# Kernel optimization log

Hardware: AMD Instinct MI355X
Metric: run time of the kernel (lower is better)

Reference implementation:

```python
import jax, jax.numpy as jnp
import numpy as np

B, T, H = 2, 512, 256


def setup_inputs() -> dict:
    key = jax.random.key(0)
    k1, k2, k3, k4, k5 = jax.random.split(key, 5)
    scale = 1.0 / np.sqrt(H)
    Q = jax.random.normal(k1, (B, T, H), dtype=jnp.float32)
    K = jax.random.normal(k2, (B, T, H), dtype=jnp.float32)
    # torch nn.Linear weights: y = x @ W.T, W shape [out, in]
    Wq = jax.random.normal(k3, (H, H), dtype=jnp.float32) * scale
    Wk = jax.random.normal(k4, (H, H), dtype=jnp.float32) * scale
    v = jax.random.normal(k5, (H,), dtype=jnp.float32) * scale  # Linear(H,1) weight
    return {"Q": Q, "K": K, "Wq": Wq, "Wk": Wk, "v": v}


def reference(Q, K, Wq, Wk, v):
    # Project queries and keys: [B,T,H]
    Qp = jnp.einsum("bth,oh->bto", Q, Wq)
    Kp = jnp.einsum("bsh,oh->bso", K, Wk)
    # Additive (Bahdanau) scores: tanh over broadcast sum -> [B,T,T,H], then v-proj -> [B,T,T]
    e = jnp.tanh(Qp[:, :, None, :] + Kp[:, None, :, :])
    scores = jnp.einsum("btsh,h->bts", e, v)
    # Causal mask: query t may only attend to keys s <= t
    mask = jnp.tril(jnp.ones((T, T), dtype=bool))
    scores = jnp.where(mask[None, :, :], scores, jnp.float32(-1e9))
    alpha = jax.nn.softmax(scores, axis=-1)
    # Weighted sum of (raw) K values: [B,T,H]
    ctx = jnp.einsum("bts,bsh->bth", alpha, K)
    return ctx, alpha
```

## Files before the change

kernel.cpp:

```cpp
#include <hip/hip_runtime.h>

#define BB 2
#define TT 512
#define HH 256
#define NBT (BB * TT)

#define C2LOG2E 2.8853900817779268f
#define LOG2E   1.4426950408889634f

__global__ __launch_bounds__(256) void prep_T(
    const float* __restrict__ Wq, const float* __restrict__ Wk,
    float* __restrict__ WqT, float* __restrict__ WkT)
{
    int bid = blockIdx.x;
    int tid = threadIdx.x;
    const float* W = (bid < 16) ? Wq : Wk;
    float* WT = (bid < 16) ? WqT : WkT;
    int tile = bid & 15;
    int o0 = (tile >> 2) * 64, h0 = (tile & 3) * 64;
    __shared__ float t_sh[64][65];
    int ty = tid >> 6, tx = tid & 63;
#pragma unroll
    for (int r = 0; r < 16; ++r) {
        int o = r * 4 + ty;
        t_sh[o][tx] = W[(o0 + o) * HH + h0 + tx];
    }
    __syncthreads();
#pragma unroll
    for (int r = 0; r < 16; ++r) {
        int h = r * 4 + ty;
        WT[(h0 + h) * HH + o0 + tx] = t_sh[tx][h];
    }
}

__global__ __launch_bounds__(256) void proj_outer(
    const float* __restrict__ Q, const float* __restrict__ K,
    const float* __restrict__ WqT, const float* __restrict__ WkT,
    float* __restrict__ Eq, float* __restrict__ EkT)
{
    __shared__ float x_sh[8][HH];
    __shared__ float ek_sh[4][8][68];

    int bid = blockIdx.x;
    bool isK = (bid >= 128);
    int bt0 = (bid & 127) * 8;
    const float* X = isK ? K : Q;
    const float* WT = isK ? WkT : WqT;
    int tid = threadIdx.x;
    int wv = tid >> 6, lane = tid & 63;
    int o = wv * 64 + lane;

#pragma unroll
    for (int p = 0; p < 2; ++p) {
        int fi = p * 256 + tid;
        int r = fi >> 6, c = fi & 63;
        *reinterpret_cast<float4*>(&x_sh[r][c * 4]) =
            *reinterpret_cast<const float4*>(X + (bt0 + r) * HH + c * 4);
    }
    __syncthreads();

    float acc[8] = {0.f, 0.f, 0.f, 0.f, 0.f, 0.f, 0.f, 0.f};
    const float* wcol = WT + o;
#pragma unroll 2
    for (int h4 = 0; h4 < 64; ++h4) {
        float w0 = wcol[(h4 * 4 + 0) * HH];
        float w1 = wcol[(h4 * 4 + 1) * HH];
        float w2 = wcol[(h4 * 4 + 2) * HH];
        float w3 = wcol[(h4 * 4 + 3) * HH];
#pragma unroll
        for (int r = 0; r < 8; ++r) {
            float4 x4 = *reinterpret_cast<const float4*>(&x_sh[r][h4 * 4]);
            float a = acc[r];
            a = __builtin_fmaf(x4.x, w0, a);
            a = __builtin_fmaf(x4.y, w1, a);
            a = __builtin_fmaf(x4.z, w2, a);
            a = __builtin_fmaf(x4.w, w3, a);
            acc[r] = a;
        }
    }

    float e[8];
#pragma unroll
    for (int r = 0; r < 8; ++r)
        e[r] = __builtin_amdgcn_exp2f(acc[r] * C2LOG2E);

    if (!isK) {
#pragma unroll
        for (int r = 0; r < 8; ++r)
            Eq[(bt0 + r) * HH + o] = e[r];
    } else {
#pragma unroll
        for (int r = 0; r < 8; ++r)
            ek_sh[wv][r][lane] = e[r];
#pragma unroll
        for (int p = 0; p < 2; ++p) {
            int id = p * 64 + lane;
            int s = id >> 3, r = id & 7;
            float4 val = *reinterpret_cast<const float4*>(&ek_sh[wv][r][s * 4]);
            *reinterpret_cast<float4*>(
                EkT + ((wv * 16 + s) * NBT + bt0 + r) * 4) = val;
        }
    }
}

__global__ __launch_bounds__(512, 8) void attn_kernel(
    const float* __restrict__ Eq, const float* __restrict__ EkT,
    const float* __restrict__ Kraw, const float* __restrict__ v,
    float* __restrict__ ctx, float* __restrict__ alpha)
{
    __shared__ float eq_sh[HH];
    __shared__ float v2_sh[HH];
    __shared__ float al_sh[TT];
    __shared__ float red[8];
    __shared__ float4 cred[8][64];

    int bt = blockIdx.x;
    int b = bt / TT;
    int idx = bt % TT;
    int t = (idx < 256) ? idx : 767 - idx;
    int btr = b * TT + t;
    int tid = threadIdx.x;

    if (tid < HH) {
        eq_sh[tid] = Eq[btr * HH + tid];
        v2_sh[tid] = -2.0f * v[tid];
    }
    __syncthreads();

    float sc = 0.f;
    if (tid <= t) {
        const float4* ek = reinterpret_cast<const float4*>(EkT) + (b * TT + tid);
        const float4* q4p = reinterpret_cast<const float4*>(eq_sh);
        const float4* v4p = reinterpret_cast<const float4*>(v2_sh);
#pragma unroll 4
        for (int h4 = 0; h4 < HH / 4; ++h4) {
            float4 e4 = ek[h4 * NBT];
            float4 q4 = q4p[h4];
            float4 vv = v4p[h4];
            float r0 = __builtin_amdgcn_rcpf(__builtin_fmaf(q4.x, e4.x, 1.f));
            float r1 = __builtin_amdgcn_rcpf(__builtin_fmaf(q4.y, e4.y, 1.f));
            float r2 = __builtin_amdgcn_rcpf(__builtin_fmaf(q4.z, e4.z, 1.f));
            float r3 = __builtin_amdgcn_rcpf(__builtin_fmaf(q4.w, e4.w, 1.f));
            sc = __builtin_fmaf(vv.x, r0, sc);
            sc = __builtin_fmaf(vv.y, r1, sc);
            sc = __builtin_fmaf(vv.z, r2, sc);
            sc = __builtin_fmaf(vv.w, r3, sc);
        }
    }

    float e = (tid <= t) ? __builtin_amdgcn_exp2f(sc * LOG2E) : 0.f;
    float ssum = e;
#pragma unroll
    for (int off = 32; off > 0; off >>= 1)
        ssum += __shfl_xor(ssum, off);
    if ((tid & 63) == 0) red[tid >> 6] = ssum;
    __syncthreads();
    float denom = (red[0] + red[1]) + (red[2] + red[3])
                + (red[4] + red[5]) + (red[6] + red[7]);
    float a0 = e * __builtin_amdgcn_rcpf(denom);

    al_sh[tid] = a0;
    alpha[btr * TT + tid] = a0;
    __syncthreads();

    int hc = tid & 63, sg = tid >> 6;
    const float4* kb4 = reinterpret_cast<const float4*>(Kraw + b * TT * HH) + hc;
    float4 acc4 = {0.f, 0.f, 0.f, 0.f};
    for (int s = sg; s <= t; s += 8) {
        float4 k4 = kb4[s * 64];
        float  al = al_sh[s];
        acc4.x = __builtin_fmaf(al, k4.x, acc4.x);
        acc4.y = __builtin_fmaf(al, k4.y, acc4.y);
        acc4.z = __builtin_fmaf(al, k4.z, acc4.z);
        acc4.w = __builtin_fmaf(al, k4.w, acc4.w);
    }
    cred[sg][hc] = acc4;
    __syncthreads();
    if (sg == 0) {
        float4 out = {0.f, 0.f, 0.f, 0.f};
#pragma unroll
        for (int g = 0; g < 8; ++g) {
            float4 cc = cred[g][hc];
            out.x += cc.x; out.y += cc.y; out.z += cc.z; out.w += cc.w;
        }
        reinterpret_cast<float4*>(ctx + btr * HH)[hc] = out;
    }
}

extern "C" void kernel_launch(void* const* d_in, const int* in_sizes, int n_in,
                              void* d_out, int out_size, void* d_ws, size_t ws_size,
                              hipStream_t stream) {
    const float* Q  = (const float*)d_in[0];
    const float* K  = (const float*)d_in[1];
    const float* Wq = (const float*)d_in[2];
    const float* Wk = (const float*)d_in[3];
    const float* v  = (const float*)d_in[4];

    float* ctx   = (float*)d_out;
    float* alpha = (float*)d_out + NBT * HH;

    float* Eq  = (float*)d_ws;
    float* EkT = Eq + NBT * HH;
    float* WqT = EkT + NBT * HH;
    float* WkT = WqT + HH * HH;

    prep_T<<<32, 256, 0, stream>>>(Wq, Wk, WqT, WkT);
    proj_outer<<<256, 256, 0, stream>>>(Q, K, WqT, WkT, Eq, EkT);
    attn_kernel<<<NBT, 512, 0, stream>>>(Eq, EkT, K, v, ctx, alpha);
}
```

Before: 45.87 us.

## Retile projection kernel to 4 rows per block with float4 weight loads

Restructures the projection GEMM so each block handles 4 rows instead of 8 and each thread computes 4 adjacent output columns for one row, loading weights as float4. Grid doubles to 512 blocks, giving more parallelism across CUs for this small GEMM. The trade-off is less reuse of each weight load across rows, which increases total weight traffic from L2. The EkT transpose store is simplified to match the new tiling.

Result: slower. 51.73 us (+12.8%).

```diff
diff --git a/kernel.cpp b/kernel.cpp
--- a/kernel.cpp
+++ b/kernel.cpp
@@ -33,73 +33,71 @@
     }
 }
 
-__global__ __launch_bounds__(256) void proj_outer(
+__global__ __launch_bounds__(256) void proj2_kernel(
     const float* __restrict__ Q, const float* __restrict__ K,
     const float* __restrict__ WqT, const float* __restrict__ WkT,
     float* __restrict__ Eq, float* __restrict__ EkT)
 {
-    __shared__ float x_sh[8][HH];
-    __shared__ float ek_sh[4][8][68];
+    __shared__ float x_sh[4][HH];
+    __shared__ float ek_sh[4][HH + 4];
 
     int bid = blockIdx.x;
-    bool isK = (bid >= 128);
-    int bt0 = (bid & 127) * 8;
+    bool isK = (bid >= 256);
+    int bt0 = (bid & 255) * 4;
     const float* X = isK ? K : Q;
     const float* WT = isK ? WkT : WqT;
     int tid = threadIdx.x;
-    int wv = tid >> 6, lane = tid & 63;
-    int o = wv * 64 + lane;
-
-#pragma unroll
-    for (int p = 0; p < 2; ++p) {
-        int fi = p * 256 + tid;
-        int r = fi >> 6, c = fi & 63;
+    int q = tid & 63;
+    int rg = tid >> 6;
+
+    {
+        int r = tid >> 6, c = tid & 63;
         *reinterpret_cast<float4*>(&x_sh[r][c * 4]) =
             *reinterpret_cast<const float4*>(X + (bt0 + r) * HH + c * 4);
     }
     __syncthreads();
 
-    float acc[8] = {0.f, 0.f, 0.f, 0.f, 0.f, 0.f, 0.f, 0.f};
-    const float* wcol = WT + o;
-#pragma unroll 2
+    float4 acc = {0.f, 0.f, 0.f, 0.f};
+    const float* wbase = WT + q * 4;
+#pragma unroll 4
     for (int h4 = 0; h4 < 64; ++h4) {
-        float w0 = wcol[(h4 * 4 + 0) * HH];
-        float w1 = wcol[(h4 * 4 + 1) * HH];
-        float w2 = wcol[(h4 * 4 + 2) * HH];
-        float w3 = wcol[(h4 * 4 + 3) * HH];
-#pragma unroll
-        for (int r = 0; r < 8; ++r) {
-            float4 x4 = *reinterpret_cast<const float4*>(&x_sh[r][h4 * 4]);
-            float a = acc[r];
-            a = __builtin_fmaf(x4.x, w0, a);
-            a = __builtin_fmaf(x4.y, w1, a);
-            a = __builtin_fmaf(x4.z, w2, a);
-            a = __builtin_fmaf(x4.w, w3, a);
-            acc[r] = a;
-        }
-    }
-
-    float e[8];
-#pragma unroll
-    for (int r = 0; r < 8; ++r)
-        e[r] = __builtin_amdgcn_exp2f(acc[r] * C2LOG2E);
+        float4 x4 = *reinterpret_cast<const float4*>(&x_sh[rg][h4 * 4]);
+        float4 w0 = *reinterpret_cast<const float4*>(wbase + (h4 * 4 + 0) * HH);
+        float4 w1 = *reinterpret_cast<const float4*>(wbase + (h4 * 4 + 1) * HH);
+        float4 w2 = *reinterpret_cast<const float4*>(wbase + (h4 * 4 + 2) * HH);
+        float4 w3 = *reinterpret_cast<const float4*>(wbase + (h4 * 4 + 3) * HH);
+        acc.x = __builtin_fmaf(x4.x, w0.x, acc.x);
+        acc.y = __builtin_fmaf(x4.x, w0.y, acc.y);
+        acc.z = __builtin_fmaf(x4.x, w0.z, acc.z);
+        acc.w = __builtin_fmaf(x4.x, w0.w, acc.w);
+        acc.x = __builtin_fmaf(x4.y, w1.x, acc.x);
+        acc.y = __builtin_fmaf(x4.y, w1.y, acc.y);
+        acc.z = __builtin_fmaf(x4.y, w1.z, acc.z);
+        acc.w = __builtin_fmaf(x4.y, w1.w, acc.w);
+        acc.x = __builtin_fmaf(x4.z, w2.x, acc.x);
+        acc.y = __builtin_fmaf(x4.z, w2.y, acc.y);
+        acc.z = __builtin_fmaf(x4.z, w2.z, acc.z);
+        acc.w = __builtin_fmaf(x4.z, w2.w, acc.w);
+        acc.x = __builtin_fmaf(x4.w, w3.x, acc.x);
+        acc.y = __builtin_fmaf(x4.w, w3.y, acc.y);
+        acc.z = __builtin_fmaf(x4.w, w3.z, acc.z);
+        acc.w = __builtin_fmaf(x4.w, w3.w, acc.w);
+    }
+
+    float4 e;
+    e.x = __builtin_amdgcn_exp2f(acc.x * C2LOG2E);
+    e.y = __builtin_amdgcn_exp2f(acc.y * C2LOG2E);
+    e.z = __builtin_amdgcn_exp2f(acc.z * C2LOG2E);
+    e.w = __builtin_amdgcn_exp2f(acc.w * C2LOG2E);
 
     if (!isK) {
-#pragma unroll
-        for (int r = 0; r < 8; ++r)
-            Eq[(bt0 + r) * HH + o] = e[r];
+        *reinterpret_cast<float4*>(Eq + (bt0 + rg) * HH + q * 4) = e;
     } else {
-#pragma unroll
-        for (int r = 0; r < 8; ++r)
-            ek_sh[wv][r][lane] = e[r];
-#pragma unroll
-        for (int p = 0; p < 2; ++p) {
-            int id = p * 64 + lane;
-            int s = id >> 3, r = id & 7;
-            float4 val = *reinterpret_cast<const float4*>(&ek_sh[wv][r][s * 4]);
-            *reinterpret_cast<float4*>(
-                EkT + ((wv * 16 + s) * NBT + bt0 + r) * 4) = val;
-        }
+        *reinterpret_cast<float4*>(&ek_sh[rg][q * 4]) = e;
+        __syncthreads();
+        int s = tid >> 2, r = tid & 3;
+        float4 val = *reinterpret_cast<const float4*>(&ek_sh[r][s * 4]);
+        *reinterpret_cast<float4*>(EkT + (s * NBT + bt0 + r) * 4) = val;
     }
 }
 
@@ -205,6 +203,6 @@
     float* WkT = WqT + HH * HH;
 
     prep_T<<<32, 256, 0, stream>>>(Wq, Wk, WqT, WkT);
-    proj_outer<<<256, 256, 0, stream>>>(Q, K, WqT, WkT, Eq, EkT);
+    proj2_kernel<<<512, 256, 0, stream>>>(Q, K, WqT, WkT, Eq, EkT);
     attn_kernel<<<NBT, 512, 0, stream>>>(Eq, EkT, K, v, ctx, alpha);
 }
```
